# Optimization experiments

Hardware: AMD Instinct MI355X
Metric: run time of the kernel (lower is better)

The kernel has to match this reference:

```python
import jax, jax.numpy as jnp
import numpy as np

N = 50000        # nodes
E = 800000       # edges (before self-loops)
IN = 512         # in_channels
HEADS = 8        # 'head' arg: heads and per-head out dim of conv1
C1 = 8           # per-head channels of conv1 (== head)
OUT = 128        # out_channels of conv2
NEG_SLOPE = 0.2  # PyG GATConv leaky-relu slope


def _glorot(key, shape, fan_in):
    return jax.random.normal(key, shape, jnp.float32) * (1.0 / np.sqrt(fan_in))


def setup_inputs() -> dict:
    key = jax.random.key(0)
    ks = jax.random.split(key, 10)
    x = jax.random.normal(ks[0], (N, IN), jnp.float32)
    edge_index = jax.random.randint(ks[1], (2, E), 0, N, dtype=jnp.int32)
    # conv1: GATConv(IN, C1, heads=HEADS, concat=True)
    W1 = _glorot(ks[2], (IN, HEADS * C1), IN)
    att_src1 = _glorot(ks[3], (HEADS, C1), C1)
    att_dst1 = _glorot(ks[4], (HEADS, C1), C1)
    bias1 = jnp.zeros((HEADS * C1,), jnp.float32)
    # conv2: GATConv(HEADS*C1, OUT, heads=1, concat=False)
    W2 = _glorot(ks[5], (HEADS * C1, OUT), HEADS * C1)
    att_src2 = _glorot(ks[6], (1, OUT), OUT)
    att_dst2 = _glorot(ks[7], (1, OUT), OUT)
    bias2 = jnp.zeros((OUT,), jnp.float32)
    return {"x": x, "edge_index": edge_index,
            "W1": W1, "att_src1": att_src1, "att_dst1": att_dst1, "bias1": bias1,
            "W2": W2, "att_src2": att_src2, "att_dst2": att_dst2, "bias2": bias2}


def gat_conv(x, src, dst, W, a_src, a_dst, bias, heads, concat):
    """PyG GATConv (eval mode, dropout off). src/dst already include self-loops."""
    n = x.shape[0]
    h = (x @ W).reshape(n, heads, -1)                 # [N, H, C]
    s = (h * a_src[None]).sum(-1)                     # [N, H] alpha_src per node
    d = (h * a_dst[None]).sum(-1)                     # [N, H] alpha_dst per node
    alpha = jax.nn.leaky_relu(s[src] + d[dst], NEG_SLOPE)  # [E, H]
    # segment softmax over incoming edges of each destination node
    amax = jax.ops.segment_max(alpha, dst, num_segments=n)  # [N, H]
    amax = jnp.where(jnp.isfinite(amax), amax, 0.0)
    ea = jnp.exp(alpha - amax[dst])                   # [E, H]
    denom = jax.ops.segment_sum(ea, dst, num_segments=n)
    w = ea / (denom[dst] + 1e-16)                     # [E, H]
    msg = h[src] * w[..., None]                       # [E, H, C]
    out = jax.ops.segment_sum(msg, dst, num_segments=n)  # [N, H, C]
    out = out.reshape(n, -1) if concat else out.mean(axis=1)
    return out + bias


def reference(x, edge_index, W1, att_src1, att_dst1, bias1,
              W2, att_src2, att_dst2, bias2):
    n = x.shape[0]
    loop = jnp.arange(n, dtype=edge_index.dtype)      # PyG adds self-loops
    src = jnp.concatenate([edge_index[0], loop])
    dst = jnp.concatenate([edge_index[1], loop])
    h = jax.nn.elu(gat_conv(x, src, dst, W1, att_src1, att_dst1, bias1,
                            heads=HEADS, concat=True))
    out = jax.nn.elu(gat_conv(h, src, dst, W2, att_src2, att_dst2, bias2,
                              heads=1, concat=False))
    return out
```

## Files before the change

kernel.cpp:

```cpp
#include <hip/hip_runtime.h>

#define NEG_SLOPE 0.2f
#define CAP 128

typedef __attribute__((ext_vector_type(8))) short bf16x8;
typedef __attribute__((ext_vector_type(4))) float f32x4;

__device__ __forceinline__ float leaky(float v) {
    return v > 0.0f ? v : NEG_SLOPE * v;
}
__device__ __forceinline__ float elu(float v) {
    return v > 0.0f ? v : (__expf(v) - 1.0f);
}
__device__ __forceinline__ short f2b(float f) {
    return (short)((__float_as_uint(f) + 0x8000u) >> 16);
}
__device__ __forceinline__ float bf2f(unsigned short v) {
    return __uint_as_float(((unsigned)v) << 16);
}

__global__ void prep_k(const float* __restrict__ W1, const float* __restrict__ W2,
                       unsigned short* __restrict__ w1s, unsigned short* __restrict__ w2s,
                       int* __restrict__ wp, int N) {
    int i = blockIdx.x * 256 + threadIdx.x;
    if (i < N) wp[i] = 0;
    if (i < 512 * 64) {
        int k = i >> 6, n = i & 63;
        int kt = k >> 5, kk = k & 31;
        int nt = n >> 4, nn = n & 15;
        int lane = (kk >> 3) * 16 + nn, j = kk & 7;
        w1s[(((size_t)(kt * 4 + nt)) * 64 + lane) * 8 + j] = (unsigned short)f2b(W1[i]);
    } else if (i < 512 * 64 + 64 * 128) {
        int i2 = i - 512 * 64;
        int k = i2 >> 7, n = i2 & 127;
        int kt = k >> 5, kk = k & 31;
        int nt = n >> 4, nn = n & 15;
        int lane = (kk >> 3) * 16 + nn, j = kk & 7;
        w2s[(((size_t)(kt * 8 + nt)) * 64 + lane) * 8 + j] = (unsigned short)f2b(W2[i2]);
    }
}

__global__ __launch_bounds__(256) void gemm1_k(const float* __restrict__ X,
                                               const unsigned short* __restrict__ Ws,
                                               const float* __restrict__ Asrc,
                                               const float* __restrict__ Adst,
                                               unsigned short* __restrict__ Hb,
                                               float* __restrict__ S,
                                               float* __restrict__ D, int N) {
    const int lane = threadIdx.x & 63;
    const int wave = threadIdx.x >> 6;
    const int m0 = blockIdx.x * 64 + wave * 16;
    const int q = lane >> 4, lc = lane & 15;
    const int arow = m0 + lc;
    const float* xrow = X + (size_t)min(arow, N - 1) * 512 + q * 8;
    const bf16x8* bW = (const bf16x8*)Ws;

    f32x4 acc[4] = {{0.f,0.f,0.f,0.f},{0.f,0.f,0.f,0.f},{0.f,0.f,0.f,0.f},{0.f,0.f,0.f,0.f}};

    for (int g = 0; g < 2; ++g) {
        float4 a[16];
#pragma unroll
        for (int u = 0; u < 16; ++u)
            a[u] = *(const float4*)(xrow + g * 256 + (u >> 1) * 32 + (u & 1) * 4);
#pragma unroll
        for (int u2 = 0; u2 < 8; ++u2) {
            const int kt = g * 8 + u2;
            float4 a0 = a[u2 * 2], a1 = a[u2 * 2 + 1];
            bf16x8 af;
            af[0] = f2b(a0.x); af[1] = f2b(a0.y); af[2] = f2b(a0.z); af[3] = f2b(a0.w);
            af[4] = f2b(a1.x); af[5] = f2b(a1.y); af[6] = f2b(a1.z); af[7] = f2b(a1.w);
#pragma unroll
            for (int nt = 0; nt < 4; ++nt) {
                bf16x8 bf = bW[(size_t)(kt * 4 + nt) * 64 + lane];
                acc[nt] = __builtin_amdgcn_mfma_f32_16x16x32_bf16(af, bf, acc[nt], 0, 0, 0);
            }
        }
    }

    float asc[4], adc[4];
#pragma unroll
    for (int nt = 0; nt < 4; ++nt) { asc[nt] = Asrc[nt * 16 + lc]; adc[nt] = Adst[nt * 16 + lc]; }

#pragma unroll
    for (int r = 0; r < 4; ++r) {
        int row = m0 + q * 4 + r;
        bool ok = row < N;
        if (ok) {
#pragma unroll
            for (int nt = 0; nt < 4; ++nt)
                Hb[(size_t)row * 64 + nt * 16 + lc] = (unsigned short)f2b(acc[nt][r]);
        }
        float ps[4], pd[4];
#pragma unroll
        for (int nt = 0; nt < 4; ++nt) { ps[nt] = acc[nt][r] * asc[nt]; pd[nt] = acc[nt][r] * adc[nt]; }
#pragma unroll
        for (int off = 1; off < 8; off <<= 1) {
#pragma unroll
            for (int nt = 0; nt < 4; ++nt) {
                ps[nt] += __shfl_xor(ps[nt], off);
                pd[nt] += __shfl_xor(pd[nt], off);
            }
        }
        if (ok && !(lc & 7)) {
            int hb = lc >> 3;
#pragma unroll
            for (int nt = 0; nt < 4; ++nt) {
                S[(size_t)row * 8 + nt * 2 + hb] = ps[nt];
                D[(size_t)row * 8 + nt * 2 + hb] = pd[nt];
            }
        }
    }
}

__global__ __launch_bounds__(256) void pack_k(const int* __restrict__ ei, int E,
                                              int* __restrict__ wp, int* __restrict__ srcs) {
    int e = blockIdx.x * 256 + threadIdx.x;
    if (e < E) {
        int s = ei[e];
        int d = ei[E + e];
        int c = atomicAdd(&wp[d], 1);
        if (c < CAP) srcs[((size_t)d << 7) + c] = s;
    }
}

__global__ __launch_bounds__(256) void agg1g2_k(const int* __restrict__ wp,
                                                const int* __restrict__ srcs,
                                                const float* __restrict__ S1,
                                                const float* __restrict__ D1,
                                                const unsigned short* __restrict__ H1b,
                                                const float* __restrict__ b1,
                                                const unsigned short* __restrict__ W2s,
                                                const float* __restrict__ as2,
                                                const float* __restrict__ ad2,
                                                unsigned short* __restrict__ H2b,
                                                float* __restrict__ S2,
                                                float* __restrict__ D2, int N) {
    __shared__ unsigned short sh[16][64];
    __shared__ float shp[4][16], shq[4][16];

    const int tid  = threadIdx.x;
    const int lane = tid & 63;
    const int wave = tid >> 6;
    const int m0 = blockIdx.x * 16;

    const int h = lane & 7;
    const int eg = lane >> 3;
#pragma unroll
    for (int rep = 0; rep < 4; ++rep) {
        const int nl = wave * 4 + rep;
        const int wid = m0 + nl;
        if (wid < N) {
            const int deg = min(wp[wid], CAP);
            const size_t b0 = (size_t)wid << 7;
            const float dvh = D1[(size_t)wid * 8 + h];

            float wself = __expf(leaky(S1[(size_t)wid * 8 + h] + dvh));
            float den = (eg == 0) ? wself : 0.0f;
            float acc[8] = {0.f,0.f,0.f,0.f,0.f,0.f,0.f,0.f};
            if (eg == 0) {
                bf16x8 hv = *(const bf16x8*)(H1b + (size_t)wid * 64 + h * 8);
#pragma unroll
                for (int c = 0; c < 8; ++c)
                    acc[c] = wself * bf2f((unsigned short)hv[c]);
            }

            for (int base = 0; base < deg; base += 8) {
                int i = base + eg;
                bool v = i < deg;
                int src = v ? srcs[b0 + i] : wid;
                float w = v ? __expf(leaky(S1[(size_t)src * 8 + h] + dvh)) : 0.0f;
                den += w;
                bf16x8 hv = *(const bf16x8*)(H1b + (size_t)src * 64 + h * 8);
#pragma unroll
                for (int c = 0; c < 8; ++c)
                    acc[c] += w * bf2f((unsigned short)hv[c]);
            }
#pragma unroll
            for (int off = 8; off < 64; off <<= 1) {
                den += __shfl_xor(den, off);
#pragma unroll
                for (int c = 0; c < 8; ++c)
                    acc[c] += __shfl_xor(acc[c], off);
            }
            if (eg == 0) {
                const float rden = 1.0f / (den + 1e-16f);
                bf16x8 o;
#pragma unroll
                for (int c = 0; c < 8; ++c)
                    o[c] = f2b(elu(acc[c] * rden + b1[h * 8 + c]));
                *(bf16x8*)(&sh[nl][h * 8]) = o;
            }
        } else if (eg == 0) {
            *(bf16x8*)(&sh[nl][h * 8]) = bf16x8{0,0,0,0,0,0,0,0};
        }
    }
    __syncthreads();

    const int q = lane >> 4, lc = lane & 15;
    const bf16x8* bW = (const bf16x8*)W2s;
    const int nt0 = wave * 2;

    f32x4 acc2[2] = {{0.f,0.f,0.f,0.f},{0.f,0.f,0.f,0.f}};
#pragma unroll
    for (int kt = 0; kt < 2; ++kt) {
        bf16x8 af = *(const bf16x8*)(&sh[lc][q * 8 + kt * 32]);
#pragma unroll
        for (int u = 0; u < 2; ++u) {
            bf16x8 bf = bW[(size_t)(kt * 8 + nt0 + u) * 64 + lane];
            acc2[u] = __builtin_amdgcn_mfma_f32_16x16x32_bf16(af, bf, acc2[u], 0, 0, 0);
        }
    }
    float asc[2], adc[2];
#pragma unroll
    for (int u = 0; u < 2; ++u) {
        asc[u] = as2[(nt0 + u) * 16 + lc];
        adc[u] = ad2[(nt0 + u) * 16 + lc];
    }
#pragma unroll
    for (int r = 0; r < 4; ++r) {
        int rl = q * 4 + r;
        int row = m0 + rl;
        if (row < N) {
#pragma unroll
            for (int u = 0; u < 2; ++u)
                H2b[(size_t)row * 128 + (nt0 + u) * 16 + lc] = (unsigned short)f2b(acc2[u][r]);
        }
        float ps = acc2[0][r] * asc[0] + acc2[1][r] * asc[1];
        float pd = acc2[0][r] * adc[0] + acc2[1][r] * adc[1];
#pragma unroll
        for (int off = 1; off < 16; off <<= 1) {
            ps += __shfl_xor(ps, off);
            pd += __shfl_xor(pd, off);
        }
        if (lc == 0) { shp[wave][rl] = ps; shq[wave][rl] = pd; }
    }
    __syncthreads();
    if (tid < 16) {
        int row = m0 + tid;
        if (row < N) {
            float s = shp[0][tid] + shp[1][tid] + shp[2][tid] + shp[3][tid];
            float d = shq[0][tid] + shq[1][tid] + shq[2][tid] + shq[3][tid];
            S2[row] = s;
            D2[row] = d;
        }
    }
}

__global__ __launch_bounds__(256) void agg2_k(const int* __restrict__ wp,
                                              const int* __restrict__ srcs,
                                              const float* __restrict__ S,
                                              const float* __restrict__ D,
                                              const unsigned short* __restrict__ Hb,
                                              const float* __restrict__ bias,
                                              float* __restrict__ out, int N) {
    const int wid = (blockIdx.x * 256 + threadIdx.x) >> 6;
    const int lane = threadIdx.x & 63;
    if (wid >= N) return;
    const int deg = min(wp[wid], CAP);
    const size_t b0 = (size_t)wid << 7;
    const float dv = D[wid];
    const int c0 = lane * 2;

    const float wself = __expf(leaky(S[wid] + dv));
    float den = (lane == 0) ? wself : 0.0f;
    float acc0, acc1;
    {
        unsigned pv = *(const unsigned*)(Hb + (size_t)wid * 128 + c0);
        acc0 = wself * __uint_as_float(pv << 16);
        acc1 = wself * __uint_as_float(pv & 0xffff0000u);
    }

    for (int base = 0; base < deg; base += 64) {
        int i = base + lane;
        int src_l = 0; float w_l = 0.0f;
        if (i < deg) {
            src_l = srcs[b0 + i];
            w_l = __expf(leaky(S[src_l] + dv));
        }
        den += w_l;
        const int cnt = min(64, deg - base);
        for (int j0 = 0; j0 < cnt; j0 += 8) {
#pragma unroll
            for (int u = 0; u < 8; ++u) {
                int j = j0 + u;
                float w = __shfl(w_l, j);
                int src = __builtin_amdgcn_readfirstlane(__shfl(src_l, j));
                unsigned pv = *(const unsigned*)(Hb + (size_t)src * 128 + c0);
                acc0 += w * __uint_as_float(pv << 16);
                acc1 += w * __uint_as_float(pv & 0xffff0000u);
            }
        }
    }
#pragma unroll
    for (int off = 1; off < 64; off <<= 1)
        den += __shfl_xor(den, off);
    const float rden = 1.0f / (den + 1e-16f);
    float2 o;
    o.x = elu(acc0 * rden + bias[c0]);
    o.y = elu(acc1 * rden + bias[c0 + 1]);
    *(float2*)(out + (size_t)wid * 128 + c0) = o;
}

extern "C" void kernel_launch(void* const* d_in, const int* in_sizes, int n_in,
                              void* d_out, int out_size, void* d_ws, size_t ws_size,
                              hipStream_t stream) {
    const float* x   = (const float*)d_in[0];
    const int*   ei  = (const int*)d_in[1];
    const float* W1  = (const float*)d_in[2];
    const float* as1 = (const float*)d_in[3];
    const float* ad1 = (const float*)d_in[4];
    const float* b1  = (const float*)d_in[5];
    const float* W2  = (const float*)d_in[6];
    const float* as2 = (const float*)d_in[7];
    const float* ad2 = (const float*)d_in[8];
    const float* b2  = (const float*)d_in[9];

    const int N = in_sizes[0] / 512;
    const int E = in_sizes[1] / 2;

    unsigned short* w1s  = (unsigned short*)d_ws;
    unsigned short* w2s  = w1s + 512 * 64;
    unsigned short* h1b  = w2s + 64 * 128;
    unsigned short* h2b  = h1b + (size_t)N * 64;
    float*          s1   = (float*)(h2b + (size_t)N * 128);
    float*          d1   = s1 + (size_t)N * 8;
    float*          s2   = d1 + (size_t)N * 8;
    float*          d2   = s2 + N;
    int*            wp   = (int*)(d2 + N);
    int*            srcs = wp + N;

    const int B = 256;
    const int gblk = (N + 63) / 64;
    int prep_n = 512 * 64 + 64 * 128;
    if (N > prep_n) prep_n = N;

    prep_k<<<(prep_n + B - 1) / B, B, 0, stream>>>(W1, W2, w1s, w2s, wp, N);
    gemm1_k<<<gblk, B, 0, stream>>>(x, w1s, as1, ad1, h1b, s1, d1, N);
    pack_k<<<(E + B - 1) / B, B, 0, stream>>>(ei, E, wp, srcs);
    agg1g2_k<<<(N + 15) / 16, B, 0, stream>>>(wp, srcs, s1, d1, h1b, b1,
                                              w2s, as2, ad2, h2b, s2, d2, N);
    agg2_k<<<(N + 3) / 4, B, 0, stream>>>(wp, srcs, s2, d2, h2b, b2,
                                          (float*)d_out, N);
}
```

Baseline: 317.9 us.

## Process eight edges in parallel per wave in layer-2 aggregation

Restructures the layer-2 aggregation so each wave splits into 8 edge groups of 8 lanes, with each lane loading 16 bf16 channels via two 16-byte vector loads. Previously the wave walked edges one at a time, with every lane loading 4 bytes. The change is meant to raise memory-level parallelism and cut per-edge shuffle and readfirstlane overhead. In exchange it adds a cross-group shuffle reduction of 16 accumulators, raises register pressure, and leaves only 8 lanes active for the final writes.

```diff
diff --git a/kernel.cpp b/kernel.cpp
--- a/kernel.cpp
+++ b/kernel.cpp
@@ -259,46 +259,61 @@
     const int deg = min(wp[wid], CAP);
     const size_t b0 = (size_t)wid << 7;
     const float dv = D[wid];
-    const int c0 = lane * 2;
+    const int eg = lane >> 3;
+    const int sl = lane & 7;
+    const int c0 = sl * 16;
 
     const float wself = __expf(leaky(S[wid] + dv));
-    float den = (lane == 0) ? wself : 0.0f;
-    float acc0, acc1;
-    {
-        unsigned pv = *(const unsigned*)(Hb + (size_t)wid * 128 + c0);
-        acc0 = wself * __uint_as_float(pv << 16);
-        acc1 = wself * __uint_as_float(pv & 0xffff0000u);
-    }
-
-    for (int base = 0; base < deg; base += 64) {
-        int i = base + lane;
-        int src_l = 0; float w_l = 0.0f;
-        if (i < deg) {
-            src_l = srcs[b0 + i];
-            w_l = __expf(leaky(S[src_l] + dv));
-        }
-        den += w_l;
-        const int cnt = min(64, deg - base);
-        for (int j0 = 0; j0 < cnt; j0 += 8) {
-#pragma unroll
-            for (int u = 0; u < 8; ++u) {
-                int j = j0 + u;
-                float w = __shfl(w_l, j);
-                int src = __builtin_amdgcn_readfirstlane(__shfl(src_l, j));
-                unsigned pv = *(const unsigned*)(Hb + (size_t)src * 128 + c0);
-                acc0 += w * __uint_as_float(pv << 16);
-                acc1 += w * __uint_as_float(pv & 0xffff0000u);
-            }
+    float den = (eg == 0) ? wself : 0.0f;
+    float acc[16] = {0.f,0.f,0.f,0.f,0.f,0.f,0.f,0.f,
+                     0.f,0.f,0.f,0.f,0.f,0.f,0.f,0.f};
+    if (eg == 0) {
+        bf16x8 hv0 = *(const bf16x8*)(Hb + (size_t)wid * 128 + c0);
+        bf16x8 hv1 = *(const bf16x8*)(Hb + (size_t)wid * 128 + c0 + 8);
+#pragma unroll
+        for (int c = 0; c < 8; ++c) {
+            acc[c]     = wself * bf2f((unsigned short)hv0[c]);
+            acc[c + 8] = wself * bf2f((unsigned short)hv1[c]);
+        }
+    }
+
+    for (int base = 0; base < deg; base += 8) {
+        int i = base + eg;
+        bool v = i < deg;
+        int src = v ? srcs[b0 + i] : wid;
+        float w = v ? __expf(leaky(S[src] + dv)) : 0.0f;
+        den += w;
+        bf16x8 hv0 = *(const bf16x8*)(Hb + (size_t)src * 128 + c0);
+        bf16x8 hv1 = *(const bf16x8*)(Hb + (size_t)src * 128 + c0 + 8);
+#pragma unroll
+        for (int c = 0; c < 8; ++c) {
+            acc[c]     += w * bf2f((unsigned short)hv0[c]);
+            acc[c + 8] += w * bf2f((unsigned short)hv1[c]);
         }
     }
 #pragma unroll
     for (int off = 1; off < 64; off <<= 1)
         den += __shfl_xor(den, off);
-    const float rden = 1.0f / (den + 1e-16f);
-    float2 o;
-    o.x = elu(acc0 * rden + bias[c0]);
-    o.y = elu(acc1 * rden + bias[c0 + 1]);
-    *(float2*)(out + (size_t)wid * 128 + c0) = o;
+#pragma unroll
+    for (int off = 8; off < 64; off <<= 1) {
+#pragma unroll
+        for (int c = 0; c < 16; ++c)
+            acc[c] += __shfl_xor(acc[c], off);
+    }
+    if (eg == 0) {
+        const float rden = 1.0f / (den * 0.125f + 1e-16f);
+        float4 o[4];
+#pragma unroll
+        for (int u = 0; u < 4; ++u) {
+            o[u].x = elu(acc[u * 4 + 0] * rden + bias[c0 + u * 4 + 0]);
+            o[u].y = elu(acc[u * 4 + 1] * rden + bias[c0 + u * 4 + 1]);
+            o[u].z = elu(acc[u * 4 + 2] * rden + bias[c0 + u * 4 + 2]);
+            o[u].w = elu(acc[u * 4 + 3] * rden + bias[c0 + u * 4 + 3]);
+        }
+#pragma unroll
+        for (int u = 0; u < 4; ++u)
+            *(float4*)(out + (size_t)wid * 128 + c0 + u * 4) = o[u];
+    }
 }
 
 extern "C" void kernel_launch(void* const* d_in, const int* in_sizes, int n_in,
```

Result: slower. 327.6 us (+3.0%).
